# Optimization experiments

Hardware: AMD Instinct MI355X
Metric: run time of the kernel (lower is better)

Reference implementation:

```python
import jax, jax.numpy as jnp
import numpy as np

N = 50000      # nodes
E = 800000     # edges (before self-loops)
F_IN = 128     # num_node_features
H = 4          # heads
C = 32         # graph_hidden_channels (per head)
HC = H * C     # 128
NHID = 512
NOUT = 768
G = 256        # graphs in batch
NEG_SLOPE = 0.2


def setup_inputs() -> dict:
    key = jax.random.key(0)
    ks = jax.random.split(key, 32)
    s = 0.05
    inp = {
        "x": jax.random.normal(ks[0], (N, F_IN), jnp.float32),
        "edge_index": jax.random.randint(ks[1], (2, E), 0, N, jnp.int64),
        "batch": jnp.sort(jax.random.randint(ks[2], (N,), 0, G, jnp.int64)),
    }
    dims = [F_IN, HC, HC]
    k = 3
    for i, din in enumerate(dims, start=1):
        inp[f"w{i}"] = jax.random.normal(ks[k], (din, HC), jnp.float32) * s; k += 1
        inp[f"as{i}"] = jax.random.normal(ks[k], (H, C), jnp.float32) * s; k += 1
        inp[f"ad{i}"] = jax.random.normal(ks[k], (H, C), jnp.float32) * s; k += 1
        inp[f"b{i}"] = jnp.zeros((HC,), jnp.float32)
        inp[f"sk{i}w"] = jax.random.normal(ks[k], (din, HC), jnp.float32) * s; k += 1
        inp[f"sk{i}b"] = jnp.zeros((HC,), jnp.float32)
    inp["m1w"] = jax.random.normal(ks[k], (HC, NHID), jnp.float32) * s; k += 1
    inp["m1b"] = jnp.zeros((NHID,), jnp.float32)
    inp["m2w"] = jax.random.normal(ks[k], (NHID, NOUT), jnp.float32) * s
    inp["m2b"] = jnp.zeros((NOUT,), jnp.float32)
    return inp


def _gat_conv(x, src, dst, W, a_src, a_dst, b):
    # x: [N, din]; src/dst: [E+N] (self-loops included)
    n = x.shape[0]
    h = (x @ W).reshape(n, H, C)                       # [N, H, C]
    e_src = jnp.sum(h * a_src, axis=-1)                # [N, H]
    e_dst = jnp.sum(h * a_dst, axis=-1)                # [N, H]
    e = jax.nn.leaky_relu(e_src[src] + e_dst[dst], NEG_SLOPE)  # [E', H]
    m = jax.ops.segment_max(e, dst, num_segments=n)    # segment softmax (stable)
    ex = jnp.exp(e - m[dst])
    z = jax.ops.segment_sum(ex, dst, num_segments=n)
    alpha = ex / z[dst]                                # [E', H]
    out = jax.ops.segment_sum(alpha[:, :, None] * h[src], dst, num_segments=n)
    return out.reshape(n, HC) + b


def reference(x, edge_index, batch,
              w1, as1, ad1, b1, sk1w, sk1b,
              w2, as2, ad2, b2, sk2w, sk2b,
              w3, as3, ad3, b3, sk3w, sk3b,
              m1w, m1b, m2w, m2b):
    n = x.shape[0]
    loops = jnp.arange(n, dtype=edge_index.dtype)
    src = jnp.concatenate([edge_index[0], loops])      # PyG add_self_loops=True
    dst = jnp.concatenate([edge_index[1], loops])

    h = jax.nn.relu(x @ sk1w + sk1b + _gat_conv(x, src, dst, w1, as1, ad1, b1))
    h = jax.nn.relu(h @ sk2w + sk2b + _gat_conv(h, src, dst, w2, as2, ad2, b2))
    h = jax.nn.relu(h @ sk3w + sk3b + _gat_conv(h, src, dst, w3, as3, ad3, b3))

    pooled = jax.ops.segment_max(h, batch, num_segments=G)  # global_max_pool
    pooled = jnp.where(jnp.isfinite(pooled), pooled, 0.0)   # guard empty graphs
    out = jax.nn.relu(pooled @ m1w + m1b)
    out = out @ m2w + m2b
    return out
```

## Files before the change

kernel.cpp:

```cpp
#include <hip/hip_runtime.h>
#include <hip/hip_bf16.h>
#include <math.h>

#define NN 50000
#define EE 800000
#define EPE 850000
#define HCC 128
#define GGR 256
#define NHIDD 512
#define NOUTD 768
#define CHUNK 256
#define SCAN_NBLK ((NN + 1023) / 1024)
#define MBLK ((NN + 63) / 64)

typedef __attribute__((ext_vector_type(8))) short bf16x8;
typedef __attribute__((ext_vector_type(4))) float f32x4;

__device__ __forceinline__ void atomicMaxF(float* addr, float v) {
    if (v >= 0.f) atomicMax(reinterpret_cast<int*>(addr), __float_as_int(v));
    else atomicMin(reinterpret_cast<unsigned int*>(addr), __float_as_uint(v));
}

__device__ __forceinline__ float lrelu(float x) { return x > 0.f ? x : 0.2f * x; }

__device__ __forceinline__ ushort f2bf(float f) {
    unsigned u = __float_as_uint(f);
    unsigned r = (u + 0x7fffu + ((u >> 16) & 1u)) >> 16;
    return (ushort)r;
}
__device__ __forceinline__ float bf2f(ushort b) {
    return __uint_as_float(((unsigned)b) << 16);
}

__global__ void conv_x(const float* __restrict__ X, ushort* __restrict__ Xb) {
    int i = blockIdx.x * 256 + threadIdx.x;
    if (i < NN * HCC / 4) {
        float4 v = reinterpret_cast<const float4*>(X)[i];
        ushort4 o;
        o.x = f2bf(v.x); o.y = f2bf(v.y); o.z = f2bf(v.z); o.w = f2bf(v.w);
        reinterpret_cast<ushort4*>(Xb)[i] = o;
    }
}

__global__ void conv_w(const float* __restrict__ W, const float* __restrict__ SKW,
                       ushort* __restrict__ Wt) {
    int i = blockIdx.x * 256 + threadIdx.x;
    if (i >= 256 * 128) return;
    int n = i >> 7, k = i & 127;
    float v = (n < 128) ? W[(size_t)k * 128 + n] : SKW[(size_t)k * 128 + (n - 128)];
    Wt[i] = f2bf(v);
}

__global__ void hist_zero(int* __restrict__ counts) {
    int i = blockIdx.x * 256 + threadIdx.x;
    if (i < NN) counts[i] = 0;
}

__global__ void hist(const int* __restrict__ ei, int* __restrict__ counts) {
    int e = blockIdx.x * 256 + threadIdx.x;
    if (e >= EPE) return;
    int d = (e < EE) ? ei[EE + e] : e - EE;
    atomicAdd(&counts[d], 1);
}

__global__ __launch_bounds__(256) void scan_partial(const int* __restrict__ counts,
                                                    int* __restrict__ excl,
                                                    int* __restrict__ blocksums)
{
    __shared__ int s[256];
    const int b = blockIdx.x, t = threadIdx.x;
    const int idx = b * 1024 + t * 4;
    int a0 = (idx + 0 < NN) ? counts[idx + 0] : 0;
    int a1 = (idx + 1 < NN) ? counts[idx + 1] : 0;
    int a2 = (idx + 2 < NN) ? counts[idx + 2] : 0;
    int a3 = (idx + 3 < NN) ? counts[idx + 3] : 0;
    int sum4 = a0 + a1 + a2 + a3;
    s[t] = sum4;
    __syncthreads();
    #pragma unroll
    for (int off = 1; off < 256; off <<= 1) {
        int add = (t >= off) ? s[t - off] : 0;
        __syncthreads();
        s[t] += add;
        __syncthreads();
    }
    int e0 = s[t] - sum4;
    if (idx + 0 < NN) excl[idx + 0] = e0;
    if (idx + 1 < NN) excl[idx + 1] = e0 + a0;
    if (idx + 2 < NN) excl[idx + 2] = e0 + a0 + a1;
    if (idx + 3 < NN) excl[idx + 3] = e0 + a0 + a1 + a2;
    if (t == 255) blocksums[b] = s[255];
}

__global__ __launch_bounds__(64) void scan_sums(int* __restrict__ blocksums,
                                                int* __restrict__ blockoffs,
                                                int* __restrict__ row_start)
{
    __shared__ int s[64];
    int t = threadIdx.x;
    int v = (t < SCAN_NBLK) ? blocksums[t] : 0;
    s[t] = v;
    __syncthreads();
    #pragma unroll
    for (int off = 1; off < 64; off <<= 1) {
        int add = (t >= off) ? s[t - off] : 0;
        __syncthreads();
        s[t] += add;
        __syncthreads();
    }
    if (t < SCAN_NBLK) blockoffs[t] = s[t] - v;
    if (t == 63) row_start[NN] = s[63];
}

__global__ void scan_add(const int* __restrict__ excl, const int* __restrict__ blockoffs,
                         int* __restrict__ row_start, int* __restrict__ cursor)
{
    int i = blockIdx.x * 256 + threadIdx.x;
    if (i >= NN) return;
    int v = excl[i] + blockoffs[i >> 10];
    row_start[i] = v;
    cursor[i] = v;
}

__global__ void scatter_csr(const int* __restrict__ ei, int* __restrict__ cursor,
                            int* __restrict__ csr_src) {
    int e = blockIdx.x * 256 + threadIdx.x;
    if (e >= EPE) return;
    int s, d;
    if (e < EE) { s = ei[e]; d = ei[EE + e]; } else { s = d = e - EE; }
    int pos = atomicAdd(&cursor[d], 1);
    csr_src[pos] = s;
}

__global__ __launch_bounds__(256) void gemm_mfma(
    const ushort* __restrict__ Xb,
    const ushort* __restrict__ Wt,
    const float* __restrict__ skb, const float* __restrict__ bb,
    ushort* __restrict__ Hout, float* __restrict__ Agg)
{
    __shared__ ushort Xs[64 * 128];
    const int r0 = blockIdx.x * 64;
    const int tid = threadIdx.x;
    const int w = tid >> 6;
    const int l = tid & 63;
    const int lm = l & 15;
    const int lk = l >> 4;

    #pragma unroll
    for (int it = 0; it < 4; ++it) {
        int slot = it * 256 + tid;
        int row = slot >> 4;
        int bc = (slot & 15) << 4;
        int n = r0 + row;
        bf16x8 v = (bf16x8)(short)0;
        if (n < NN) v = *reinterpret_cast<const bf16x8*>(Xb + (size_t)n * 128 + (bc >> 1));
        *reinterpret_cast<bf16x8*>(reinterpret_cast<char*>(Xs) + row * 256 + (bc ^ ((row & 7) << 4))) = v;
    }
    __syncthreads();

    f32x4 acc[4][4];
    #pragma unroll
    for (int nb = 0; nb < 4; ++nb)
        #pragma unroll
        for (int rf = 0; rf < 4; ++rf)
            acc[nb][rf] = (f32x4){0.f, 0.f, 0.f, 0.f};

    #pragma unroll
    for (int ks = 0; ks < 4; ++ks) {
        bf16x8 a[4];
        #pragma unroll
        for (int rf = 0; rf < 4; ++rf) {
            int row = rf * 16 + lm;
            int bc = (ks * 32 + lk * 8) * 2;
            a[rf] = *reinterpret_cast<const bf16x8*>(
                reinterpret_cast<const char*>(Xs) + row * 256 + (bc ^ ((row & 7) << 4)));
        }
        #pragma unroll
        for (int nb = 0; nb < 4; ++nb) {
            int ncol = (w * 4 + nb) * 16 + lm;
            bf16x8 b = *reinterpret_cast<const bf16x8*>(Wt + (size_t)ncol * 128 + ks * 32 + lk * 8);
            #pragma unroll
            for (int rf = 0; rf < 4; ++rf)
                acc[nb][rf] = __builtin_amdgcn_mfma_f32_16x16x32_bf16(a[rf], b, acc[nb][rf], 0, 0, 0);
        }
    }

    #pragma unroll
    for (int nb = 0; nb < 4; ++nb) {
        int ncol = (w * 4 + nb) * 16 + lm;
        #pragma unroll
        for (int rf = 0; rf < 4; ++rf) {
            #pragma unroll
            for (int r = 0; r < 4; ++r) {
                int n = r0 + rf * 16 + lk * 4 + r;
                if (n >= NN) continue;
                float v = acc[nb][rf][r];
                if (ncol < 128) {
                    Hout[(size_t)n * 128 + ncol] = f2bf(v);
                } else {
                    int c = ncol - 128;
                    Agg[(size_t)n * 128 + c] = v + skb[c] + bb[c];
                }
            }
        }
    }
}

__global__ __launch_bounds__(256) void node_attn(
    const ushort* __restrict__ Hb, const float* __restrict__ as_, const float* __restrict__ ad_,
    float* __restrict__ esrc, float* __restrict__ edst)
{
    int tid = threadIdx.x;
    int node = blockIdx.x * 2 + (tid >> 7);
    int t = tid & 127;
    if (node >= NN) return;
    float hv = bf2f(Hb[(size_t)node * 128 + t]);
    float p1 = hv * as_[t];
    float p2 = hv * ad_[t];
    #pragma unroll
    for (int o = 16; o > 0; o >>= 1) {
        p1 += __shfl_down(p1, o, 32);
        p2 += __shfl_down(p2, o, 32);
    }
    if ((t & 31) == 0) {
        esrc[node * 4 + (t >> 5)] = p1;
        edst[node * 4 + (t >> 5)] = p2;
    }
}

__global__ __launch_bounds__(128) void gat_aggr(
    const int* __restrict__ row_start, const int* __restrict__ csr_src,
    const float* __restrict__ esrc, const float* __restrict__ edst,
    const ushort* __restrict__ Hb, const float* __restrict__ skipagg,
    ushort* __restrict__ outbuf)
{
    __shared__ int   lsrc[CHUNK];
    __shared__ float lw[CHUNK * 4];
    const int d = blockIdx.x;
    const int t = threadIdx.x;
    const int hd = t >> 5;
    const int l = t & 31;
    const int r0 = row_start[d], r1 = row_start[d + 1];
    const float4 edv = *reinterpret_cast<const float4*>(edst + (size_t)d * 4);
    float acc = 0.f;
    float m_h = -INFINITY, z_h = 0.f;

    for (int base = r0; base < r1; base += CHUNK) {
        const int nc = min(CHUNK, r1 - base);
        __syncthreads();
        for (int i = t; i < nc; i += 128) {
            int s = csr_src[base + i];
            lsrc[i] = s;
            float4 ev = *reinterpret_cast<const float4*>(esrc + (size_t)s * 4);
            lw[i * 4 + 0] = lrelu(ev.x + edv.x);
            lw[i * 4 + 1] = lrelu(ev.y + edv.y);
            lw[i * 4 + 2] = lrelu(ev.z + edv.z);
            lw[i * 4 + 3] = lrelu(ev.w + edv.w);
        }
        __syncthreads();
        float mx = m_h;
        for (int i = l; i < nc; i += 32) mx = fmaxf(mx, lw[i * 4 + hd]);
        #pragma unroll
        for (int off = 16; off > 0; off >>= 1) mx = fmaxf(mx, __shfl_xor(mx, off, 32));
        float sc = __expf(m_h - mx);
        float zp = 0.f;
        for (int i = l; i < nc; i += 32) {
            float w = __expf(lw[i * 4 + hd] - mx);
            lw[i * 4 + hd] = w;
            zp += w;
        }
        #pragma unroll
        for (int off = 16; off > 0; off >>= 1) zp += __shfl_xor(zp, off, 32);
        z_h = z_h * sc + zp;
        m_h = mx;
        acc *= sc;
        __syncthreads();
        #pragma unroll 4
        for (int i = 0; i < nc; ++i) {
            acc += lw[i * 4 + hd] * bf2f(Hb[(size_t)lsrc[i] * 128 + t]);
        }
    }
    float res = skipagg[(size_t)d * 128 + t] + acc / z_h;
    outbuf[(size_t)d * 128 + t] = f2bf(fmaxf(res, 0.f));
}

__global__ void pool_init(float* __restrict__ pooled) {
    int i = blockIdx.x * 256 + threadIdx.x;
    if (i < GGR * HCC) pooled[i] = -INFINITY;
}

__global__ void pool_max(const ushort* __restrict__ xf, const int* __restrict__ batch,
                         float* __restrict__ pooled)
{
    int i = blockIdx.x * 256 + threadIdx.x;
    if (i >= NN * HCC) return;
    int n = i >> 7, c = i & 127;
    atomicMaxF(&pooled[batch[n] * 128 + c], bf2f(xf[i]));
}

__global__ __launch_bounds__(512) void mlp1(const float* __restrict__ pooled,
                                            const float* __restrict__ w,
                                            const float* __restrict__ bias,
                                            float* __restrict__ hid)
{
    __shared__ float xs[128];
    int g = blockIdx.x, t = threadIdx.x;
    if (t < 128) {
        float v = pooled[g * 128 + t];
        if (!isfinite(v)) v = 0.f;
        xs[t] = v;
    }
    __syncthreads();
    float acc = 0.f;
    #pragma unroll 8
    for (int k = 0; k < 128; ++k) acc += xs[k] * w[(size_t)k * NHIDD + t];
    hid[(size_t)g * NHIDD + t] = fmaxf(acc + bias[t], 0.f);
}

__global__ __launch_bounds__(768) void mlp2(const float* __restrict__ hid,
                                            const float* __restrict__ w,
                                            const float* __restrict__ bias,
                                            float* __restrict__ out)
{
    __shared__ float xs[NHIDD];
    int g = blockIdx.x, t = threadIdx.x;
    if (t < NHIDD) xs[t] = hid[(size_t)g * NHIDD + t];
    __syncthreads();
    float acc = 0.f;
    #pragma unroll 8
    for (int k = 0; k < NHIDD; ++k) acc += xs[k] * w[(size_t)k * NOUTD + t];
    out[(size_t)g * NOUTD + t] = acc + bias[t];
}

extern "C" void kernel_launch(void* const* d_in, const int* in_sizes, int n_in,
                              void* d_out, int out_size, void* d_ws, size_t ws_size,
                              hipStream_t stream)
{
    const float* x = (const float*)d_in[0];
    const int* ei = (const int*)d_in[1];
    const int* batch = (const int*)d_in[2];
    const float* W[3]   = {(const float*)d_in[3],  (const float*)d_in[9],  (const float*)d_in[15]};
    const float* AS[3]  = {(const float*)d_in[4],  (const float*)d_in[10], (const float*)d_in[16]};
    const float* AD[3]  = {(const float*)d_in[5],  (const float*)d_in[11], (const float*)d_in[17]};
    const float* B[3]   = {(const float*)d_in[6],  (const float*)d_in[12], (const float*)d_in[18]};
    const float* SKW[3] = {(const float*)d_in[7],  (const float*)d_in[13], (const float*)d_in[19]};
    const float* SKB[3] = {(const float*)d_in[8],  (const float*)d_in[14], (const float*)d_in[20]};
    const float* m1w = (const float*)d_in[21];
    const float* m1b = (const float*)d_in[22];
    const float* m2w = (const float*)d_in[23];
    const float* m2b = (const float*)d_in[24];
    float* out = (float*)d_out;

    float* p = (float*)d_ws;
    ushort* bufA = (ushort*)p; p += (size_t)NN * HCC / 2;
    ushort* bufB = (ushort*)p; p += (size_t)NN * HCC / 2;
    ushort* xb   = (ushort*)p; p += (size_t)NN * HCC / 2;
    ushort* hbuf = (ushort*)p; p += (size_t)NN * HCC / 2;
    ushort* wt3  = (ushort*)p; p += 3 * 256 * 128 / 2;
    float* agg  = p; p += (size_t)NN * HCC;
    float* esrc = p; p += NN * 4;
    float* edst = p; p += NN * 4;
    float* pooled = p; p += GGR * HCC;
    float* hidden = p; p += GGR * NHIDD;
    int* counts    = (int*)p; p += NN;
    int* excl      = (int*)p; p += NN;
    int* row_start = (int*)p; p += NN + 4;
    int* cursor    = (int*)p; p += NN;
    int* csr_src   = (int*)p; p += EPE;
    int* blocksums = (int*)p; p += 64;
    int* blockoffs = (int*)p; p += 64;

    conv_x<<<(NN * HCC / 4 + 255) / 256, 256, 0, stream>>>(x, xb);
    for (int l = 0; l < 3; ++l)
        conv_w<<<(256 * 128 + 255) / 256, 256, 0, stream>>>(W[l], SKW[l], wt3 + l * 256 * 128);

    hist_zero<<<(NN + 255) / 256, 256, 0, stream>>>(counts);
    hist<<<(EPE + 255) / 256, 256, 0, stream>>>(ei, counts);
    scan_partial<<<SCAN_NBLK, 256, 0, stream>>>(counts, excl, blocksums);
    scan_sums<<<1, 64, 0, stream>>>(blocksums, blockoffs, row_start);
    scan_add<<<(NN + 255) / 256, 256, 0, stream>>>(excl, blockoffs, row_start, cursor);
    scatter_csr<<<(EPE + 255) / 256, 256, 0, stream>>>(ei, cursor, csr_src);

    const ushort* cur = xb;
    ushort* outs[3] = {bufA, bufB, bufA};
    for (int l = 0; l < 3; ++l) {
        gemm_mfma<<<MBLK, 256, 0, stream>>>(cur, wt3 + l * 256 * 128, SKB[l], B[l], hbuf, agg);
        node_attn<<<NN / 2, 256, 0, stream>>>(hbuf, AS[l], AD[l], esrc, edst);
        gat_aggr<<<NN, 128, 0, stream>>>(row_start, csr_src, esrc, edst, hbuf, agg, outs[l]);
        cur = outs[l];
    }
    pool_init<<<(GGR * HCC) / 256, 256, 0, stream>>>(pooled);
    pool_max<<<(NN * HCC + 255) / 256, 256, 0, stream>>>(cur, batch, pooled);
    mlp1<<<GGR, NHIDD, 0, stream>>>(pooled, m1w, m1b, hidden);
    mlp2<<<GGR, NOUTD, 0, stream>>>(hidden, m2w, m2b, out);
}
```

Measured before the change: 582.5 us.

## Vectorize GAT aggregation gathers with 16-byte bf16 loads across edge slots

The aggregation kernel no longer has each thread load one bf16 element per edge. Each group of 16 threads now reads a full 256-byte source row with 16-byte vector loads, and the 8 thread groups handle different edges in parallel. Partial sums go into a shared buffer and are reduced at the end. The attention weight array is also moved to a head-major padded layout to avoid bank conflicts. This cuts load instruction count and exposes more memory-level parallelism, at the cost of more registers, extra shared memory and a final reduction step.

```diff
diff --git a/kernel.cpp b/kernel.cpp
--- a/kernel.cpp
+++ b/kernel.cpp
@@ -10,6 +10,7 @@
 #define NHIDD 512
 #define NOUTD 768
 #define CHUNK 256
+#define CPAD (CHUNK + 8)
 #define SCAN_NBLK ((NN + 1023) / 1024)
 #define MBLK ((NN + 63) / 64)
 
@@ -235,14 +236,20 @@
     ushort* __restrict__ outbuf)
 {
     __shared__ int   lsrc[CHUNK];
-    __shared__ float lw[CHUNK * 4];
+    __shared__ float lw[4][CPAD];
+    __shared__ float shsc[4];
+    __shared__ float accbuf[8][HCC];
     const int d = blockIdx.x;
     const int t = threadIdx.x;
     const int hd = t >> 5;
     const int l = t & 31;
+    const int slot = t >> 4;
+    const int cg = t & 15;
+    const int c0 = cg * 8;
+    const int ghd = cg >> 2;
     const int r0 = row_start[d], r1 = row_start[d + 1];
     const float4 edv = *reinterpret_cast<const float4*>(edst + (size_t)d * 4);
-    float acc = 0.f;
+    float acc[8] = {0.f, 0.f, 0.f, 0.f, 0.f, 0.f, 0.f, 0.f};
     float m_h = -INFINITY, z_h = 0.f;
 
     for (int base = r0; base < r1; base += CHUNK) {
@@ -252,35 +259,48 @@
             int s = csr_src[base + i];
             lsrc[i] = s;
             float4 ev = *reinterpret_cast<const float4*>(esrc + (size_t)s * 4);
-            lw[i * 4 + 0] = lrelu(ev.x + edv.x);
-            lw[i * 4 + 1] = lrelu(ev.y + edv.y);
-            lw[i * 4 + 2] = lrelu(ev.z + edv.z);
-            lw[i * 4 + 3] = lrelu(ev.w + edv.w);
+            lw[0][i] = lrelu(ev.x + edv.x);
+            lw[1][i] = lrelu(ev.y + edv.y);
+            lw[2][i] = lrelu(ev.z + edv.z);
+            lw[3][i] = lrelu(ev.w + edv.w);
         }
         __syncthreads();
         float mx = m_h;
-        for (int i = l; i < nc; i += 32) mx = fmaxf(mx, lw[i * 4 + hd]);
+        for (int i = l; i < nc; i += 32) mx = fmaxf(mx, lw[hd][i]);
         #pragma unroll
         for (int off = 16; off > 0; off >>= 1) mx = fmaxf(mx, __shfl_xor(mx, off, 32));
         float sc = __expf(m_h - mx);
         float zp = 0.f;
         for (int i = l; i < nc; i += 32) {
-            float w = __expf(lw[i * 4 + hd] - mx);
-            lw[i * 4 + hd] = w;
+            float w = __expf(lw[hd][i] - mx);
+            lw[hd][i] = w;
             zp += w;
         }
         #pragma unroll
         for (int off = 16; off > 0; off >>= 1) zp += __shfl_xor(zp, off, 32);
         z_h = z_h * sc + zp;
         m_h = mx;
-        acc *= sc;
-        __syncthreads();
-        #pragma unroll 4
-        for (int i = 0; i < nc; ++i) {
-            acc += lw[i * 4 + hd] * bf2f(Hb[(size_t)lsrc[i] * 128 + t]);
-        }
-    }
-    float res = skipagg[(size_t)d * 128 + t] + acc / z_h;
+        if (l == 0) shsc[hd] = sc;
+        __syncthreads();
+        float scg = shsc[ghd];
+        #pragma unroll
+        for (int j = 0; j < 8; ++j) acc[j] *= scg;
+        for (int i = slot; i < nc; i += 8) {
+            int s = lsrc[i];
+            float wgt = lw[ghd][i];
+            bf16x8 row = *reinterpret_cast<const bf16x8*>(Hb + (size_t)s * 128 + c0);
+            #pragma unroll
+            for (int j = 0; j < 8; ++j)
+                acc[j] = fmaf(wgt, bf2f((ushort)row[j]), acc[j]);
+        }
+    }
+    #pragma unroll
+    for (int j = 0; j < 8; ++j) accbuf[slot][c0 + j] = acc[j];
+    __syncthreads();
+    float tot = 0.f;
+    #pragma unroll
+    for (int s = 0; s < 8; ++s) tot += accbuf[s][t];
+    float res = skipagg[(size_t)d * 128 + t] + tot / z_h;
     outbuf[(size_t)d * 128 + t] = f2bf(fmaxf(res, 0.f));
 }
 
```

Measured after the change: 545.3 us. 1.07x faster.
